# Optimization experiments

Hardware: AMD Instinct MI355X
Metric: run time of the kernel (lower is better)

## Reference

```python
import jax, jax.numpy as jnp
import numpy as np
import math

H, HKV, HD, HID = 32, 8, 128, 4096
ROPE_BASE = 10000.0

def rotate_half(x):
    x1, x2 = jnp.split(x, 2, axis=-1)
    return jnp.concatenate([-x2, x1], axis=-1)

def setup_inputs() -> dict:
    key = jax.random.key(0)
    ks = jax.random.split(key, 6)
    B, S = 1, 2048
    s = 0.02
    return {
        "hidden_states": jax.random.normal(ks[0], (B, S, HID), jnp.float32),
        "position_ids": jnp.arange(S, dtype=jnp.int64)[None, :].repeat(B, axis=0),
        # weights stored as [in, out] (transpose of torch Linear weight)
        "wq": jax.random.normal(ks[1], (HID, H * HD), jnp.float32) * s,
        "wk": jax.random.normal(ks[2], (HID, HKV * HD), jnp.float32) * s,
        "wv": jax.random.normal(ks[3], (HID, HKV * HD), jnp.float32) * s,
        "wo": jax.random.normal(ks[4], (H * HD, HID), jnp.float32) * s,
    }

def reference(hidden_states, position_ids, wq, wk, wv, wo):
    B, S, _ = hidden_states.shape
    g = H // HKV
    # projections
    q = (hidden_states @ wq).reshape(B, S, H, HD).transpose(0, 2, 1, 3)    # [B,H,S,D]
    k = (hidden_states @ wk).reshape(B, S, HKV, HD).transpose(0, 2, 1, 3)  # [B,Hkv,S,D]
    v = (hidden_states @ wv).reshape(B, S, HKV, HD).transpose(0, 2, 1, 3)
    # rotary embedding
    inv_freq = 1.0 / (ROPE_BASE ** (jnp.arange(0, HD, 2, dtype=jnp.float32) / HD))
    t = position_ids.astype(jnp.float32)                      # [B,S]
    freqs = t[..., None] * inv_freq[None, None, :]            # [B,S,D/2]
    emb = jnp.concatenate([freqs, freqs], axis=-1)            # [B,S,D]
    cos = jnp.cos(emb)[:, None, :, :]                         # [B,1,S,D]
    sin = jnp.sin(emb)[:, None, :, :]
    q = q * cos + rotate_half(q) * sin
    k = k * cos + rotate_half(k) * sin
    # GQA expansion (repeat_interleave over head dim)
    k = jnp.repeat(k, g, axis=1)                              # [B,H,S,D]
    v = jnpp_repeat(v, g) if False else jnp.repeat(v, g, axis=1)
    scale = 1.0 / math.sqrt(HD)
    scores = jnp.einsum('bhqd,bhkd->bhqk', q, k) * scale      # [B,H,S,S]
    causal = jnp.triu(jnp.full((S, S), -jnp.inf, jnp.float32), k=1)
    scores = scores + causal[None, None]
    attn = jax.nn.softmax(scores.astype(jnp.float32), axis=-1).astype(q.dtype)
    out = jnp.einsum('bhqk,bhkd->bhqd', attn, v)              # [B,H,S,D]
    out = out.transpose(0, 2, 1, 3).reshape(B, S, H * HD)
    return out @ wo
```

## Files before the change

kernel.cpp:

```cpp
#include <hip/hip_runtime.h>
#include <stdint.h>

#define DHEAD 128
#define DMODEL 4096
#define NQKV 6144
#define SEQLEN 2048

typedef __attribute__((ext_vector_type(8))) short bh8;
typedef __attribute__((ext_vector_type(4))) short bh4;
typedef __attribute__((ext_vector_type(4))) float f32x4;

__device__ __forceinline__ short f2bf(float f) {
  union { float f; unsigned u; } x; x.f = f;
  unsigned r = x.u + 0x7FFFu + ((x.u >> 16) & 1u);
  return (short)(r >> 16);
}
__device__ __forceinline__ float bf2f(short s) {
  union { unsigned u; float f; } x; x.u = ((unsigned)(unsigned short)s) << 16;
  return x.f;
}
__device__ __forceinline__ void async_cp16(const void* g, void* l) {
  __builtin_amdgcn_global_load_lds((const __attribute__((address_space(1))) void*)g,
                                   (__attribute__((address_space(3))) void*)l, 16, 0, 0);
}

__global__ void cvt_bf16_kernel(const float* __restrict__ src, short* __restrict__ dst, int n) {
  int idx = (blockIdx.x * blockDim.x + threadIdx.x) * 4;
  if (idx >= n) return;
  float4 v = *(const float4*)(src + idx);
  bh4 o;
  o.x = f2bf(v.x); o.y = f2bf(v.y); o.z = f2bf(v.z); o.w = f2bf(v.w);
  *(bh4*)(dst + idx) = o;
}

__global__ void cvt_t_kernel(const float* __restrict__ src, short* __restrict__ dst, int K, int N) {
  __shared__ float tile[32][33];
  int bx = blockIdx.x * 32;
  int by = blockIdx.y * 32;
  int tx = threadIdx.x, ty = threadIdx.y;
  for (int j = 0; j < 4; j++)
    tile[ty + 8 * j][tx] = src[(size_t)(by + ty + 8 * j) * N + bx + tx];
  __syncthreads();
  for (int j = 0; j < 4; j++)
    dst[(size_t)(bx + ty + 8 * j) * K + by + tx] = f2bf(tile[tx][ty + 8 * j]);
}

__global__ void vtrans_kernel(const short* __restrict__ qkv, short* __restrict__ VT) {
  __shared__ short tile[32][33];
  int bx = blockIdx.x * 32;
  int by = blockIdx.y * 32;
  int tx = threadIdx.x, ty = threadIdx.y;
  for (int j = 0; j < 4; j++)
    tile[ty + 8 * j][tx] = qkv[(size_t)(by + ty + 8 * j) * NQKV + 5120 + bx + tx];
  __syncthreads();
  for (int j = 0; j < 4; j++)
    VT[(size_t)(bx + ty + 8 * j) * 2048 + by + tx] = tile[tx][ty + 8 * j];
}

template <typename OutT>
__global__ __launch_bounds__(256) void gemm_bt(const short* __restrict__ A, const short* __restrict__ Bt,
                                               OutT* __restrict__ C, int M, int N, int K) {
  __shared__ __align__(16) short As[128 * 32];
  __shared__ __align__(16) short Bs[128 * 32];
  const int tid = threadIdx.x;
  const int lane = tid & 63, w = tid >> 6;
  const int l15 = lane & 15, q4 = lane >> 4;
  const int m0 = blockIdx.y * 128, n0 = blockIdx.x * 128;
  const int wm = (w >> 1) * 64, wn = (w & 1) * 64;

  f32x4 acc[4][4] = {};

  for (int k0 = 0; k0 < K; k0 += 32) {
    for (int h = 0; h < 2; h++) {
      int e = (h * 256 + tid) * 8;
      int row = e >> 5, col = e & 31;
      async_cp16(A + (size_t)(m0 + row) * K + k0 + col, &As[e]);
      async_cp16(Bt + (size_t)(n0 + row) * K + k0 + col, &Bs[e]);
    }
    __syncthreads();
    bh8 af[4], bf[4];
    for (int t = 0; t < 4; t++) {
      af[t] = *(const bh8*)&As[(wm + t * 16 + l15) * 32 + q4 * 8];
      bf[t] = *(const bh8*)&Bs[(wn + t * 16 + l15) * 32 + q4 * 8];
    }
    for (int i = 0; i < 4; i++)
      for (int j = 0; j < 4; j++)
        acc[i][j] = __builtin_amdgcn_mfma_f32_16x16x32_bf16(af[i], bf[j], acc[i][j], 0, 0, 0);
    __syncthreads();
  }
  for (int i = 0; i < 4; i++)
    for (int j = 0; j < 4; j++)
      for (int r = 0; r < 4; r++) {
        int row = m0 + wm + i * 16 + q4 * 4 + r;
        int col = n0 + wn + j * 16 + l15;
        float v = acc[i][j][r];
        if constexpr (sizeof(OutT) == 2)
          ((short*)C)[(size_t)row * N + col] = f2bf(v);
        else
          C[(size_t)row * N + col] = v;
      }
}

__global__ void rope_kernel(short* __restrict__ qkv) {
  int idx = blockIdx.x * blockDim.x + threadIdx.x;
  int i = idx & 63;
  int slot = (idx >> 6) % 40;
  int row = idx / (40 * 64);
  short* p = qkv + (size_t)row * NQKV + (slot < 32 ? slot * DHEAD : 4096 + (slot - 32) * DHEAD) + i;
  float x1 = bf2f(p[0]), x2 = bf2f(p[64]);
  float inv = __expf((float)i * -0.14391156831212787f);
  float ang = (float)row * inv;
  float sn, cs;
  __sincosf(ang, &sn, &cs);
  p[0] = f2bf(x1 * cs - x2 * sn);
  p[64] = f2bf(x2 * cs + x1 * sn);
}

__global__ __launch_bounds__(256) void attn_kernel(const short* __restrict__ QKV, const short* __restrict__ VT,
                                                   short* __restrict__ O) {
  const int x = blockIdx.x;
  const int h = blockIdx.y;
  const int hkv = h >> 2;
  const int tid = threadIdx.x;
  const int lane = tid & 63, w = tid >> 6;
  const int l15 = lane & 15, q4 = lane >> 4;

  __shared__ __align__(16) short Kl[2][64 * 128];
  __shared__ __align__(16) short Vl[2][128 * 64];
  __shared__ __align__(16) short Pl[4][32 * 72];

  const bh8 ONES = {0x3F80, 0x3F80, 0x3F80, 0x3F80, 0x3F80, 0x3F80, 0x3F80, 0x3F80};
  const float SCL2 = 0.12751739343415342f;

  const int st_kr = w * 16 + ((lane >> 4) & 3);
  const int v_pb = (lane & 7) ^ ((lane >> 3) & 7);
  (void)st_kr;

  for (int phase = 0; phase < 2; phase++) {
    const int qt = phase == 0 ? (15 - x) : x;
    const int qb = qt * 128;
    const int n_kt = 2 * qt + 2;

    bh8 qf[2][4];
    for (int mi = 0; mi < 2; mi++) {
      const short* qp = QKV + (size_t)(qb + w * 32 + mi * 16 + l15) * NQKV + h * DHEAD + q4 * 8;
      for (int c = 0; c < 4; c++) qf[mi][c] = *(const bh8*)(qp + c * 32);
    }

    f32x4 O_acc[2][9] = {};

    __syncthreads();
    {
      const int kb = 0;
      for (int i = 0; i < 4; i++) {
        int r = w * 16 + i * 4 + q4;
        int db = l15 ^ (r & 15);
        async_cp16(QKV + (size_t)(kb + r) * NQKV + 4096 + hkv * DHEAD + db * 8,
                   (char*)&Kl[0][0] + (w * 256 + i * 64 + lane) * 16);
        int d = w * 32 + i * 8 + (lane >> 3);
        async_cp16(VT + (size_t)(hkv * DHEAD + d) * 2048 + kb + v_pb * 8,
                   (char*)&Vl[0][0] + (w * 256 + i * 64 + lane) * 16);
      }
    }

    for (int kt = 0; kt < n_kt; kt++) {
      const int p = kt & 1;
      const int kb = kt * 64;
      __syncthreads();
      if (kt + 1 < n_kt) {
        const int kb2 = kb + 64;
        for (int i = 0; i < 4; i++) {
          int r = w * 16 + i * 4 + q4;
          int db = l15 ^ (r & 15);
          async_cp16(QKV + (size_t)(kb2 + r) * NQKV + 4096 + hkv * DHEAD + db * 8,
                     (char*)&Kl[p ^ 1][0] + (w * 256 + i * 64 + lane) * 16);
          int d = w * 32 + i * 8 + (lane >> 3);
          async_cp16(VT + (size_t)(hkv * DHEAD + d) * 2048 + kb2 + v_pb * 8,
                     (char*)&Vl[p ^ 1][0] + (w * 256 + i * 64 + lane) * 16);
        }
      }

      const int row_base = qb + w * 32;
      const bool act0 = (kb <= row_base + 15);
      const bool act1 = (kb <= row_base + 31);
      if (act0 | act1) {
        for (int t = 0; t < 4; t++) {
          bh8 kf[4];
          for (int c = 0; c < 4; c++) {
            int sig = (c * 4 + q4) ^ l15;
            kf[c] = *(const bh8*)&Kl[p][(t * 16 + l15) * 128 + sig * 8];
          }
          for (int mi = 0; mi < 2; mi++) {
            if (!(mi ? act1 : act0)) continue;
            f32x4 a = {};
            for (int c = 0; c < 4; c++)
              a = __builtin_amdgcn_mfma_f32_16x16x32_bf16(qf[mi][c], kf[c], a, 0, 0, 0);
            int col = kb + t * 16 + l15;
            bool nm = (kb + 63 > row_base + mi * 16);
            for (int r = 0; r < 4; r++) {
              int row = row_base + mi * 16 + q4 * 4 + r;
              float pv = exp2f(a[r] * SCL2);
              if (nm && col > row) pv = 0.0f;
              Pl[w][(mi * 16 + q4 * 4 + r) * 72 + t * 16 + l15] = f2bf(pv);
            }
          }
        }

        for (int c = 0; c < 2; c++) {
          bh8 pf[2];
          if (act0) pf[0] = *(const bh8*)&Pl[w][(l15) * 72 + c * 32 + q4 * 8];
          if (act1) pf[1] = *(const bh8*)&Pl[w][(16 + l15) * 72 + c * 32 + q4 * 8];
          for (int n = 0; n < 8; n++) {
            int sig = (c * 4 + q4) ^ (l15 & 7);
            bh8 vf = *(const bh8*)&Vl[p][(n * 16 + l15) * 64 + sig * 8];
            if (act0) O_acc[0][n] = __builtin_amdgcn_mfma_f32_16x16x32_bf16(pf[0], vf, O_acc[0][n], 0, 0, 0);
            if (act1) O_acc[1][n] = __builtin_amdgcn_mfma_f32_16x16x32_bf16(pf[1], vf, O_acc[1][n], 0, 0, 0);
          }
          if (act0) O_acc[0][8] = __builtin_amdgcn_mfma_f32_16x16x32_bf16(pf[0], ONES, O_acc[0][8], 0, 0, 0);
          if (act1) O_acc[1][8] = __builtin_amdgcn_mfma_f32_16x16x32_bf16(pf[1], ONES, O_acc[1][8], 0, 0, 0);
        }
      }
    }

    for (int mi = 0; mi < 2; mi++)
      for (int r = 0; r < 4; r++) {
        float inv = 1.0f / O_acc[mi][8][r];
        int row = qb + w * 32 + mi * 16 + q4 * 4 + r;
        for (int n = 0; n < 8; n++) {
          int col = h * DHEAD + n * 16 + l15;
          O[(size_t)row * DMODEL + col] = f2bf(O_acc[mi][n][r] * inv);
        }
      }
  }
}

extern "C" void kernel_launch(void* const* d_in, const int* in_sizes, int n_in,
                              void* d_out, int out_size, void* d_ws, size_t ws_size,
                              hipStream_t stream) {
  const float* hs = (const float*)d_in[0];
  const float* wq = (const float*)d_in[2];
  const float* wk = (const float*)d_in[3];
  const float* wv = (const float*)d_in[4];
  const float* wo = (const float*)d_in[5];
  float* out = (float*)d_out;

  short* hsb = (short*)d_ws;
  short* wqkvT = hsb + (size_t)2048 * 4096;
  short* woT = wqkvT + (size_t)6144 * 4096;
  short* qkv = woT + (size_t)4096 * 4096;
  short* VT = qkv + (size_t)2048 * 6144;
  short* abuf = VT + (size_t)1024 * 2048;

  cvt_bf16_kernel<<<8192, 256, 0, stream>>>(hs, hsb, 2048 * 4096);
  cvt_t_kernel<<<dim3(128, 128), dim3(32, 8), 0, stream>>>(wq, wqkvT, 4096, 4096);
  cvt_t_kernel<<<dim3(32, 128), dim3(32, 8), 0, stream>>>(wk, wqkvT + (size_t)4096 * 4096, 4096, 1024);
  cvt_t_kernel<<<dim3(32, 128), dim3(32, 8), 0, stream>>>(wv, wqkvT + (size_t)5120 * 4096, 4096, 1024);
  cvt_t_kernel<<<dim3(128, 128), dim3(32, 8), 0, stream>>>(wo, woT, 4096, 4096);

  gemm_bt<short><<<dim3(48, 16), 256, 0, stream>>>(hsb, wqkvT, qkv, 2048, 6144, 4096);

  rope_kernel<<<20480, 256, 0, stream>>>(qkv);
  vtrans_kernel<<<dim3(32, 64), dim3(32, 8), 0, stream>>>(qkv, VT);

  attn_kernel<<<dim3(8, 32), 256, 0, stream>>>(qkv, VT, abuf);

  gemm_bt<float><<<dim3(32, 16), 256, 0, stream>>>(abuf, woT, out, 2048, 4096, 4096);
}
```

Before: 588.1 us.

## Replace 128x128 GEMM with double-buffered 256x256 tile pipelined kernel

Replaces the simple 128x128 tile GEMM (single buffer, two full barriers per 32-wide K step) with a 512-thread 256x256 tile kernel. It uses a 64-wide K step, double-buffered LDS with XOR-swizzled layout, and staged async global-to-LDS loads interleaved between MFMA quarters. It also adds setprio around MFMA bursts and explicit vmcnt waits. This is meant to hide global load latency and raise operand reuse, at the cost of 128KB LDS per block and fewer blocks (192 and 128) on a device with 256 CUs, which may underfill the GPU.

```diff
diff --git a/kernel.cpp b/kernel.cpp
--- a/kernel.cpp
+++ b/kernel.cpp
@@ -23,6 +23,9 @@
   __builtin_amdgcn_global_load_lds((const __attribute__((address_space(1))) void*)g,
                                    (__attribute__((address_space(3))) void*)l, 16, 0, 0);
 }
+
+#define BARRIER() do { asm volatile("" ::: "memory"); __builtin_amdgcn_s_barrier(); asm volatile("" ::: "memory"); } while (0)
+#define LGKM0() asm volatile("s_waitcnt lgkmcnt(0)" ::: "memory")
 
 __global__ void cvt_bf16_kernel(const float* __restrict__ src, short* __restrict__ dst, int n) {
   int idx = (blockIdx.x * blockDim.x + threadIdx.x) * 4;
@@ -58,38 +61,131 @@
 }
 
 template <typename OutT>
-__global__ __launch_bounds__(256) void gemm_bt(const short* __restrict__ A, const short* __restrict__ Bt,
-                                               OutT* __restrict__ C, int M, int N, int K) {
-  __shared__ __align__(16) short As[128 * 32];
-  __shared__ __align__(16) short Bs[128 * 32];
+__global__ __launch_bounds__(512, 2) void gemm256(const short* __restrict__ A, const short* __restrict__ Bt,
+                                                  OutT* __restrict__ C, int M, int N, int K) {
+  __shared__ __align__(16) short lds[2][2][256 * 64];
   const int tid = threadIdx.x;
   const int lane = tid & 63, w = tid >> 6;
   const int l15 = lane & 15, q4 = lane >> 4;
-  const int m0 = blockIdx.y * 128, n0 = blockIdx.x * 128;
-  const int wm = (w >> 1) * 64, wn = (w & 1) * 64;
-
-  f32x4 acc[4][4] = {};
-
-  for (int k0 = 0; k0 < K; k0 += 32) {
-    for (int h = 0; h < 2; h++) {
-      int e = (h * 256 + tid) * 8;
-      int row = e >> 5, col = e & 31;
-      async_cp16(A + (size_t)(m0 + row) * K + k0 + col, &As[e]);
-      async_cp16(Bt + (size_t)(n0 + row) * K + k0 + col, &Bs[e]);
-    }
-    __syncthreads();
-    bh8 af[4], bf[4];
-    for (int t = 0; t < 4; t++) {
-      af[t] = *(const bh8*)&As[(wm + t * 16 + l15) * 32 + q4 * 8];
-      bf[t] = *(const bh8*)&Bs[(wn + t * 16 + l15) * 32 + q4 * 8];
-    }
+  const int m0 = blockIdx.y * 256, n0 = blockIdx.x * 256;
+  const int wm = (w >> 2) * 128, wn = (w & 3) * 64;
+  const int NT = K >> 6;
+
+  char* const ldsBase = (char*)lds;
+
+  const int srow = tid >> 3;
+  const int scol = ((tid & 7) * 8) ^ ((tid & 32) ? 16 : 0);
+  const short* const Asrc = A + (size_t)m0 * K + scol;
+  const short* const Bsrc = Bt + (size_t)n0 * K + scol;
+
+  auto stageA = [&](int buf, int h, int kt) {
+    char* d = ldsBase + buf * 65536 + h * 16384 + tid * 16;
+    const short* s = Asrc + (size_t)(h * 128 + srow) * K + kt * 64;
+    async_cp16(s, d);
+    async_cp16(s + (size_t)64 * K, d + 8192);
+  };
+  auto stageB = [&](int buf, int h, int kt) {
+    char* d = ldsBase + buf * 65536 + 32768 + h * 16384 + tid * 16;
+    const short* s = Bsrc + (size_t)(h * 128 + srow) * K + kt * 64;
+    async_cp16(s, d);
+    async_cp16(s + (size_t)64 * K, d + 8192);
+  };
+
+  const int flip = (l15 & 4) ? 32 : 0;
+  const int rdA = (wm + l15) * 128;
+  const int rdB = (wn + l15) * 128;
+  const int rk0 = (q4 * 16) ^ flip;
+  const int rk1 = (64 + q4 * 16) ^ flip;
+
+  f32x4 acc[8][4] = {};
+  bh8 af[4][2], bfr[4][2];
+
+  stageA(0, 0, 0); stageA(0, 1, 0); stageB(0, 0, 0); stageB(0, 1, 0);
+  stageB(1, 0, 1); stageB(1, 1, 1); stageA(1, 0, 1);
+  asm volatile("s_waitcnt vmcnt(6)" ::: "memory");
+  BARRIER();
+
+  for (int t = 0; t < NT; ++t) {
+    const int buf = t & 1;
+    char* const Ar = ldsBase + buf * 65536;
+    char* const Br = Ar + 32768;
+
+#pragma unroll
+    for (int i = 0; i < 4; i++) {
+      af[i][0] = *(const bh8*)(Ar + rdA + i * 2048 + rk0);
+      af[i][1] = *(const bh8*)(Ar + rdA + i * 2048 + rk1);
+      bfr[i][0] = *(const bh8*)(Br + rdB + i * 2048 + rk0);
+      bfr[i][1] = *(const bh8*)(Br + rdB + i * 2048 + rk1);
+    }
+    if (t + 1 < NT) stageA(buf ^ 1, 1, t + 1);
+    BARRIER();
+    LGKM0();
+    __builtin_amdgcn_s_setprio(1);
+#pragma unroll
     for (int i = 0; i < 4; i++)
-      for (int j = 0; j < 4; j++)
-        acc[i][j] = __builtin_amdgcn_mfma_f32_16x16x32_bf16(af[i], bf[j], acc[i][j], 0, 0, 0);
-    __syncthreads();
+#pragma unroll
+      for (int j = 0; j < 2; j++) {
+        acc[i][j] = __builtin_amdgcn_mfma_f32_16x16x32_bf16(af[i][0], bfr[j][0], acc[i][j], 0, 0, 0);
+        acc[i][j] = __builtin_amdgcn_mfma_f32_16x16x32_bf16(af[i][1], bfr[j][1], acc[i][j], 0, 0, 0);
+      }
+    __builtin_amdgcn_s_setprio(0);
+    BARRIER();
+
+    if (t + 2 < NT) stageB(buf, 0, t + 2);
+    BARRIER();
+    __builtin_amdgcn_s_setprio(1);
+#pragma unroll
+    for (int i = 0; i < 4; i++)
+#pragma unroll
+      for (int j = 2; j < 4; j++) {
+        acc[i][j] = __builtin_amdgcn_mfma_f32_16x16x32_bf16(af[i][0], bfr[j][0], acc[i][j], 0, 0, 0);
+        acc[i][j] = __builtin_amdgcn_mfma_f32_16x16x32_bf16(af[i][1], bfr[j][1], acc[i][j], 0, 0, 0);
+      }
+    __builtin_amdgcn_s_setprio(0);
+    BARRIER();
+
+#pragma unroll
+    for (int i = 0; i < 4; i++) {
+      af[i][0] = *(const bh8*)(Ar + rdA + 8192 + i * 2048 + rk0);
+      af[i][1] = *(const bh8*)(Ar + rdA + 8192 + i * 2048 + rk1);
+    }
+    if (t + 2 < NT) stageB(buf, 1, t + 2);
+    BARRIER();
+    LGKM0();
+    __builtin_amdgcn_s_setprio(1);
+#pragma unroll
+    for (int i = 0; i < 4; i++)
+#pragma unroll
+      for (int j = 0; j < 2; j++) {
+        acc[4 + i][j] = __builtin_amdgcn_mfma_f32_16x16x32_bf16(af[i][0], bfr[j][0], acc[4 + i][j], 0, 0, 0);
+        acc[4 + i][j] = __builtin_amdgcn_mfma_f32_16x16x32_bf16(af[i][1], bfr[j][1], acc[4 + i][j], 0, 0, 0);
+      }
+    __builtin_amdgcn_s_setprio(0);
+    BARRIER();
+
+    if (t + 2 < NT) stageA(buf, 0, t + 2);
+    BARRIER();
+    __builtin_amdgcn_s_setprio(1);
+#pragma unroll
+    for (int i = 0; i < 4; i++)
+#pragma unroll
+      for (int j = 2; j < 4; j++) {
+        acc[4 + i][j] = __builtin_amdgcn_mfma_f32_16x16x32_bf16(af[i][0], bfr[j][0], acc[4 + i][j], 0, 0, 0);
+        acc[4 + i][j] = __builtin_amdgcn_mfma_f32_16x16x32_bf16(af[i][1], bfr[j][1], acc[4 + i][j], 0, 0, 0);
+      }
+    __builtin_amdgcn_s_setprio(0);
+    if (t + 2 < NT)
+      asm volatile("s_waitcnt vmcnt(6)" ::: "memory");
+    else
+      asm volatile("s_waitcnt vmcnt(0)" ::: "memory");
+    BARRIER();
   }
-  for (int i = 0; i < 4; i++)
+
+#pragma unroll
+  for (int i = 0; i < 8; i++)
+#pragma unroll
     for (int j = 0; j < 4; j++)
+#pragma unroll
       for (int r = 0; r < 4; r++) {
         int row = m0 + wm + i * 16 + q4 * 4 + r;
         int col = n0 + wn + j * 16 + l15;
@@ -132,9 +228,7 @@
   const bh8 ONES = {0x3F80, 0x3F80, 0x3F80, 0x3F80, 0x3F80, 0x3F80, 0x3F80, 0x3F80};
   const float SCL2 = 0.12751739343415342f;
 
-  const int st_kr = w * 16 + ((lane >> 4) & 3);
   const int v_pb = (lane & 7) ^ ((lane >> 3) & 7);
-  (void)st_kr;
 
   for (int phase = 0; phase < 2; phase++) {
     const int qt = phase == 0 ? (15 - x) : x;
@@ -257,12 +351,12 @@
   cvt_t_kernel<<<dim3(32, 128), dim3(32, 8), 0, stream>>>(wv, wqkvT + (size_t)5120 * 4096, 4096, 1024);
   cvt_t_kernel<<<dim3(128, 128), dim3(32, 8), 0, stream>>>(wo, woT, 4096, 4096);
 
-  gemm_bt<short><<<dim3(48, 16), 256, 0, stream>>>(hsb, wqkvT, qkv, 2048, 6144, 4096);
+  gemm256<short><<<dim3(24, 8), 512, 0, stream>>>(hsb, wqkvT, qkv, 2048, 6144, 4096);
 
   rope_kernel<<<20480, 256, 0, stream>>>(qkv);
   vtrans_kernel<<<dim3(32, 64), dim3(32, 8), 0, stream>>>(qkv, VT);
 
   attn_kernel<<<dim3(8, 32), 256, 0, stream>>>(qkv, VT, abuf);
 
-  gemm_bt<float><<<dim3(32, 16), 256, 0, stream>>>(abuf, woT, out, 2048, 4096, 4096);
-}
+  gemm256<float><<<dim3(16, 8), 512, 0, stream>>>(abuf, woT, out, 2048, 4096, 4096);
+}
```

Measured after the change: 607.5 us. +3.3%, slower.
